# Kernel optimization log

Measured on AMD Instinct MI355X. Metric: run time of the kernel, lower is better.

Reference implementation:

```python
import jax, jax.numpy as jnp
import numpy as np

N, E = 20000, 320000
NODE_DIM, HID, HEADS, OUT = 256, 64, 4, 50
NEG_SLOPE = 0.2  # PyG GATv2Conv default
BN_EPS = 1e-5


def setup_inputs() -> dict:
    key = jax.random.key(0)
    ks = jax.random.split(key, 16)
    s = 0.05
    inp = {
        'x': jax.random.normal(ks[0], (N, NODE_DIM), dtype=jnp.float32),
        'edge_index': jax.random.randint(ks[1], (2, E), 0, N, dtype=jnp.int64),
        # GATv2 layer 1: in=NODE_DIM, out=HID, heads=HEADS, concat
        'W1l': jax.random.normal(ks[2], (NODE_DIM, HEADS * HID), dtype=jnp.float32) * s,
        'W1r': jax.random.normal(ks[3], (NODE_DIM, HEADS * HID), dtype=jnp.float32) * s,
        'att1': jax.random.normal(ks[4], (HEADS, HID), dtype=jnp.float32) * s,
        'b1': jnp.zeros((HEADS * HID,), dtype=jnp.float32),
        'bn1_g': jnp.ones((HEADS * HID,), dtype=jnp.float32),
        'bn1_b': jnp.zeros((HEADS * HID,), dtype=jnp.float32),
        # GATv2 layer 2: in=HEADS*HID, out=HID, heads=1
        'W2l': jax.random.normal(ks[5], (HEADS * HID, HID), dtype=jnp.float32) * s,
        'W2r': jax.random.normal(ks[6], (HEADS * HID, HID), dtype=jnp.float32) * s,
        'att2': jax.random.normal(ks[7], (1, HID), dtype=jnp.float32) * s,
        'b2': jnp.zeros((HID,), dtype=jnp.float32),
        'bn2_g': jnp.ones((HID,), dtype=jnp.float32),
        'bn2_b': jnp.zeros((HID,), dtype=jnp.float32),
        # class head
        'Wc': jax.random.normal(ks[8], (HID, OUT), dtype=jnp.float32) * s,
        'bc': jnp.zeros((OUT,), dtype=jnp.float32),
    }
    return inp


def gatv2(x, src, dst, Wl, Wr, att, bias, heads, d):
    n = x.shape[0]
    xl = (x @ Wl).reshape(n, heads, d)  # source-side transform (messages)
    xr = (x @ Wr).reshape(n, heads, d)  # target-side transform
    xj = xl[src]                        # [E, H, D] gathered source feats
    xi = xr[dst]                        # [E, H, D] gathered target feats
    e = jax.nn.leaky_relu(xi + xj, NEG_SLOPE)
    score = jnp.einsum('ehd,hd->eh', e, att)   # [E, H]
    # segment softmax over incoming edges of each destination node
    m = jax.ops.segment_max(score, dst, num_segments=n)         # [N, H]
    m = jnp.where(jnp.isfinite(m), m, 0.0)
    p = jnp.exp(score - m[dst])
    denom = jax.ops.segment_sum(p, dst, num_segments=n)          # [N, H]
    alpha = p / (denom[dst] + 1e-16)
    out = jax.ops.segment_sum(alpha[:, :, None] * xj, dst, num_segments=n)  # [N, H, D]
    return out.reshape(n, heads * d) + bias


def batchnorm(x, gamma, beta):
    mu = jnp.mean(x, axis=0)
    var = jnp.var(x, axis=0)
    return (x - mu) * jax.lax.rsqrt(var + BN_EPS) * gamma + beta


def reference(x, edge_index, W1l, W1r, att1, b1, bn1_g, bn1_b,
              W2l, W2r, att2, b2, bn2_g, bn2_b, Wc, bc):
    src, dst = edge_index[0], edge_index[1]
    h = gatv2(x, src, dst, W1l, W1r, att1, b1, HEADS, HID)
    h = jax.nn.gelu(batchnorm(h, bn1_g, bn1_b), approximate=False)
    h = gatv2(h, src, dst, W2l, W2r, att2, b2, 1, HID)
    h = jax.nn.gelu(batchnorm(h, bn2_g, bn2_b), approximate=False)
    return jax.nn.log_softmax(h @ Wc + bc, axis=1)
```

## Files before the change

kernel.cpp:

```cpp
#include <hip/hip_runtime.h>
#include <math.h>

#define N_NODES 20000
#define N_EDGES 320000
#define NODE_DIM 256
#define HID 64
#define HEADS 4
#define OUTC 50
#define NEG_SLOPE 0.2f
#define BN_EPS 1e-5f
#define LOG2E 1.4426950408889634f

typedef __attribute__((ext_vector_type(8))) short short8;
typedef __attribute__((ext_vector_type(8))) unsigned short ushort8;
typedef __attribute__((ext_vector_type(4))) unsigned short ushort4v;
typedef __attribute__((ext_vector_type(4))) float f32x4;

__device__ inline unsigned short f2bf(float f) {
  unsigned u = __float_as_uint(f);
  u += 0x7fffu + ((u >> 16) & 1u);
  return (unsigned short)(u >> 16);
}

__device__ inline float bf2f(unsigned short u) {
  return __uint_as_float((unsigned)u << 16);
}

__device__ inline float gelu_exact(float v) {
  return 0.5f * v * (1.f + erff(v * 0.70710678118f));
}

__global__ void cast_all_kernel(const float* __restrict__ x, unsigned short* __restrict__ xb,
                                const float* __restrict__ W1l, const float* __restrict__ W1r,
                                const float* __restrict__ W2l, const float* __restrict__ W2r,
                                unsigned short* __restrict__ w1b,
                                unsigned short* __restrict__ w2b) {
  int i = blockIdx.x * blockDim.x + threadIdx.x;
  if (i < 1280000) {
    float4 v = ((const float4*)x)[i];
    ushort4v o = {f2bf(v.x), f2bf(v.y), f2bf(v.z), f2bf(v.w)};
    ((ushort4v*)xb)[i] = o;
  }
  if (i < 131072) {
    int k = i >> 9, j = i & 511;
    w1b[i] = f2bf(j < 256 ? W1l[k * 256 + j] : W1r[k * 256 + j - 256]);
  }
  if (i < 32768) {
    int k = i >> 7, j = i & 127;
    w2b[i] = f2bf(j < 64 ? W2l[k * 64 + j] : W2r[k * 64 + j - 64]);
  }
}

__global__ __launch_bounds__(256) void gemm_bf16_kernel(
    const unsigned short* __restrict__ A, const unsigned short* __restrict__ B,
    unsigned short* __restrict__ C, int M, int K, int N) {
  __shared__ unsigned short As[128][40];
  __shared__ unsigned short Bs[128][40];
  int tid = threadIdx.x;
  int lane = tid & 63, w = tid >> 6;
  int bm = blockIdx.y * 128, bn = blockIdx.x * 128;

  f32x4 acc[2][8] = {};

  for (int k0 = 0; k0 < K; k0 += 32) {
#pragma unroll
    for (int s = tid; s < 512; s += 256) {
      int row = s >> 2, half = s & 3;
      int gr = bm + row;
      ushort8 v = {0, 0, 0, 0, 0, 0, 0, 0};
      if (gr < M) v = *(const ushort8*)&A[(size_t)gr * K + k0 + half * 8];
      *(ushort8*)&As[row][half * 8] = v;
    }
#pragma unroll
    for (int s = tid; s < 512; s += 256) {
      int k = s >> 4, c0 = (s & 15) * 8;
      ushort8 v = *(const ushort8*)&B[(size_t)(k0 + k) * N + bn + c0];
#pragma unroll
      for (int j = 0; j < 8; j++) Bs[c0 + j][k] = v[j];
    }
    __syncthreads();

    short8 av[2], bv[8];
#pragma unroll
    for (int fr = 0; fr < 2; fr++)
      av[fr] = *(const short8*)&As[w * 32 + fr * 16 + (lane & 15)][(lane >> 4) * 8];
#pragma unroll
    for (int fc = 0; fc < 8; fc++)
      bv[fc] = *(const short8*)&Bs[fc * 16 + (lane & 15)][(lane >> 4) * 8];
#pragma unroll
    for (int fr = 0; fr < 2; fr++)
#pragma unroll
      for (int fc = 0; fc < 8; fc++)
        acc[fr][fc] = __builtin_amdgcn_mfma_f32_16x16x32_bf16(av[fr], bv[fc], acc[fr][fc], 0, 0, 0);
    __syncthreads();
  }

#pragma unroll
  for (int fr = 0; fr < 2; fr++)
#pragma unroll
    for (int fc = 0; fc < 8; fc++)
#pragma unroll
      for (int i = 0; i < 4; i++) {
        int r = bm + w * 32 + fr * 16 + (lane >> 4) * 4 + i;
        if (r < M) C[(size_t)r * N + bn + fc * 16 + (lane & 15)] = f2bf(acc[fr][fc][i]);
      }
}

__global__ void hist_kernel(const int* __restrict__ dst, int* __restrict__ deg) {
  int i = blockIdx.x * blockDim.x + threadIdx.x;
  if (i < N_EDGES) atomicAdd(&deg[dst[i]], 1);
}

__global__ void scan_kernel(const int* __restrict__ deg, int* __restrict__ rowptr) {
  __shared__ int part[1024];
  int tid = threadIdx.x;
  const int CH = (N_NODES + 1023) / 1024;
  int base = tid * CH;
  int s = 0;
  for (int i = 0; i < CH; i++) {
    int idx = base + i;
    if (idx < N_NODES) s += deg[idx];
  }
  part[tid] = s;
  __syncthreads();
  for (int off = 1; off < 1024; off <<= 1) {
    int v = (tid >= off) ? part[tid - off] : 0;
    __syncthreads();
    part[tid] += v;
    __syncthreads();
  }
  int run = (tid == 0) ? 0 : part[tid - 1];
  for (int i = 0; i < CH; i++) {
    int idx = base + i;
    if (idx < N_NODES) {
      rowptr[idx] = run;
      run += deg[idx];
    }
  }
  if (tid == 1023) rowptr[N_NODES] = run;
}

__global__ void scatter_kernel(const int* __restrict__ src, const int* __restrict__ dst,
                               const int* __restrict__ rowptr, int* __restrict__ cursor,
                               int* __restrict__ csr_src) {
  int i = blockIdx.x * blockDim.x + threadIdx.x;
  if (i < N_EDGES) {
    int d = dst[i];
    int pos = rowptr[d] + atomicAdd(&cursor[d], 1);
    csr_src[pos] = src[i];
  }
}

__global__ void agg1_kernel(const unsigned short* __restrict__ C1,
                            const float* __restrict__ att, const float* __restrict__ bias,
                            const int* __restrict__ rowptr, const int* __restrict__ csr_src,
                            float* __restrict__ out) {
  int wave = threadIdx.x >> 6;
  int lane = threadIdx.x & 63;
  int n = blockIdx.x * 4 + wave;
  if (n >= N_NODES) return;

  ushort4v xi4 = *(const ushort4v*)&C1[(size_t)n * 512 + 256 + 4 * lane];
  float xi0 = bf2f(xi4[0]), xi1 = bf2f(xi4[1]), xi2 = bf2f(xi4[2]), xi3 = bf2f(xi4[3]);
  float4 attv = *(const float4*)&att[4 * lane];
  attv.x *= LOG2E; attv.y *= LOG2E; attv.z *= LOG2E; attv.w *= LOG2E;

  float acc0 = 0.f, acc1 = 0.f, acc2 = 0.f, acc3 = 0.f;
  float lsum = 0.f;

  int e0 = rowptr[n], e1 = rowptr[n + 1];
  int e = e0;
#define EDGE_SCORE(S, T, X0, X1, X2, X3)                                              \
  {                                                                                   \
    float u0 = xi0 + X0, u1 = xi1 + X1, u2 = xi2 + X2, u3 = xi3 + X3;                 \
    T = fmaxf(u0, NEG_SLOPE * u0) * attv.x + fmaxf(u1, NEG_SLOPE * u1) * attv.y +     \
        fmaxf(u2, NEG_SLOPE * u2) * attv.z + fmaxf(u3, NEG_SLOPE * u3) * attv.w;      \
  }
  for (; e + 4 <= e1; e += 4) {
    int s0 = csr_src[e], s1 = csr_src[e + 1], s2 = csr_src[e + 2], s3 = csr_src[e + 3];
    ushort4v a4 = *(const ushort4v*)&C1[(size_t)s0 * 512 + 4 * lane];
    ushort4v b4 = *(const ushort4v*)&C1[(size_t)s1 * 512 + 4 * lane];
    ushort4v c4 = *(const ushort4v*)&C1[(size_t)s2 * 512 + 4 * lane];
    ushort4v d4 = *(const ushort4v*)&C1[(size_t)s3 * 512 + 4 * lane];
    float xa0 = bf2f(a4[0]), xa1 = bf2f(a4[1]), xa2 = bf2f(a4[2]), xa3 = bf2f(a4[3]);
    float xb0 = bf2f(b4[0]), xb1 = bf2f(b4[1]), xb2 = bf2f(b4[2]), xb3 = bf2f(b4[3]);
    float xc0 = bf2f(c4[0]), xc1 = bf2f(c4[1]), xc2 = bf2f(c4[2]), xc3 = bf2f(c4[3]);
    float xd0 = bf2f(d4[0]), xd1 = bf2f(d4[1]), xd2 = bf2f(d4[2]), xd3 = bf2f(d4[3]);

    float ta, tb, tc, td;
    EDGE_SCORE(s0, ta, xa0, xa1, xa2, xa3);
    EDGE_SCORE(s1, tb, xb0, xb1, xb2, xb3);
    EDGE_SCORE(s2, tc, xc0, xc1, xc2, xc3);
    EDGE_SCORE(s3, td, xd0, xd1, xd2, xd3);

    ta += __shfl_xor(ta, 8); tb += __shfl_xor(tb, 8); tc += __shfl_xor(tc, 8); td += __shfl_xor(td, 8);
    ta += __shfl_xor(ta, 4); tb += __shfl_xor(tb, 4); tc += __shfl_xor(tc, 4); td += __shfl_xor(td, 4);
    ta += __shfl_xor(ta, 2); tb += __shfl_xor(tb, 2); tc += __shfl_xor(tc, 2); td += __shfl_xor(td, 2);
    ta += __shfl_xor(ta, 1); tb += __shfl_xor(tb, 1); tc += __shfl_xor(tc, 1); td += __shfl_xor(td, 1);

    float pa = __builtin_amdgcn_exp2f(ta);
    float pb = __builtin_amdgcn_exp2f(tb);
    float pc = __builtin_amdgcn_exp2f(tc);
    float pd = __builtin_amdgcn_exp2f(td);
    lsum += (pa + pb) + (pc + pd);
    acc0 += pa * xa0 + pb * xb0 + pc * xc0 + pd * xd0;
    acc1 += pa * xa1 + pb * xb1 + pc * xc1 + pd * xd1;
    acc2 += pa * xa2 + pb * xb2 + pc * xc2 + pd * xd2;
    acc3 += pa * xa3 + pb * xb3 + pc * xc3 + pd * xd3;
  }
  for (; e < e1; e++) {
    int s0 = csr_src[e];
    ushort4v a4 = *(const ushort4v*)&C1[(size_t)s0 * 512 + 4 * lane];
    float xa0 = bf2f(a4[0]), xa1 = bf2f(a4[1]), xa2 = bf2f(a4[2]), xa3 = bf2f(a4[3]);
    float ta;
    EDGE_SCORE(s0, ta, xa0, xa1, xa2, xa3);
    ta += __shfl_xor(ta, 8);
    ta += __shfl_xor(ta, 4);
    ta += __shfl_xor(ta, 2);
    ta += __shfl_xor(ta, 1);
    float pa = __builtin_amdgcn_exp2f(ta);
    lsum += pa;
    acc0 += pa * xa0;
    acc1 += pa * xa1;
    acc2 += pa * xa2;
    acc3 += pa * xa3;
  }
#undef EDGE_SCORE

  float inv = 1.f / (lsum + 1e-16f);
  float4 bv = *(const float4*)&bias[4 * lane];
  float4 o;
  o.x = acc0 * inv + bv.x;
  o.y = acc1 * inv + bv.y;
  o.z = acc2 * inv + bv.z;
  o.w = acc3 * inv + bv.w;
  *(float4*)&out[(size_t)n * 256 + 4 * lane] = o;
}

__global__ void agg2_kernel(const unsigned short* __restrict__ xlr,
                            const float* __restrict__ att, const float* __restrict__ bias,
                            const int* __restrict__ rowptr, const int* __restrict__ csr_src,
                            float* __restrict__ out) {
  int wave = threadIdx.x >> 6;
  int lane = threadIdx.x & 63;
  int n = blockIdx.x * 4 + wave;
  if (n >= N_NODES) return;

  int g = lane >> 4, slot = lane & 15;
  ushort4v xi4 = *(const ushort4v*)&xlr[(size_t)n * 128 + 64 + 4 * slot];
  float xi0 = bf2f(xi4[0]), xi1 = bf2f(xi4[1]), xi2 = bf2f(xi4[2]), xi3 = bf2f(xi4[3]);
  float4 attv = *(const float4*)&att[4 * slot];
  attv.x *= LOG2E; attv.y *= LOG2E; attv.z *= LOG2E; attv.w *= LOG2E;

  float acc0 = 0.f, acc1 = 0.f, acc2 = 0.f, acc3 = 0.f;
  float lsum = 0.f;

  int e0 = rowptr[n], e1 = rowptr[n + 1];
  int nt = (e1 - e0 + 3) >> 2;
  for (int it = 0; it < nt; it++) {
    int e = e0 + it * 4 + g;
    bool valid = e < e1;
    int s = valid ? csr_src[e] : 0;
    ushort4v xj4 = *(const ushort4v*)&xlr[(size_t)s * 128 + 4 * slot];
    float xj0 = bf2f(xj4[0]), xj1 = bf2f(xj4[1]), xj2 = bf2f(xj4[2]), xj3 = bf2f(xj4[3]);
    float u0 = xi0 + xj0, u1 = xi1 + xj1, u2 = xi2 + xj2, u3 = xi3 + xj3;
    float t = fmaxf(u0, NEG_SLOPE * u0) * attv.x + fmaxf(u1, NEG_SLOPE * u1) * attv.y +
              fmaxf(u2, NEG_SLOPE * u2) * attv.z + fmaxf(u3, NEG_SLOPE * u3) * attv.w;
    t += __shfl_xor(t, 8);
    t += __shfl_xor(t, 4);
    t += __shfl_xor(t, 2);
    t += __shfl_xor(t, 1);
    float p = valid ? __builtin_amdgcn_exp2f(t) : 0.f;
    lsum += p;
    acc0 += p * xj0;
    acc1 += p * xj1;
    acc2 += p * xj2;
    acc3 += p * xj3;
  }

  acc0 += __shfl_xor(acc0, 16); acc0 += __shfl_xor(acc0, 32);
  acc1 += __shfl_xor(acc1, 16); acc1 += __shfl_xor(acc1, 32);
  acc2 += __shfl_xor(acc2, 16); acc2 += __shfl_xor(acc2, 32);
  acc3 += __shfl_xor(acc3, 16); acc3 += __shfl_xor(acc3, 32);
  lsum += __shfl_xor(lsum, 16); lsum += __shfl_xor(lsum, 32);

  if (g == 0) {
    float inv = 1.f / (lsum + 1e-16f);
    float4 bv = *(const float4*)&bias[4 * slot];
    float4 o;
    o.x = acc0 * inv + bv.x;
    o.y = acc1 * inv + bv.y;
    o.z = acc2 * inv + bv.z;
    o.w = acc3 * inv + bv.w;
    *(float4*)&out[(size_t)n * 64 + 4 * slot] = o;
  }
}

__global__ void bn_stage1_256_kernel(const float* __restrict__ x, float* __restrict__ partial) {
  int c = threadIdx.x;
  int r0 = blockIdx.x * 84;
  int r1 = min(r0 + 84, N_NODES);
  float s = 0.f, q = 0.f;
  for (int r = r0; r < r1; r++) {
    float v = x[(size_t)r * 256 + c];
    s += v;
    q += v * v;
  }
  partial[(size_t)blockIdx.x * 512 + c] = s;
  partial[(size_t)blockIdx.x * 512 + 256 + c] = q;
}

__global__ void bn_stage1_64_kernel(const float* __restrict__ x, float* __restrict__ partial) {
  __shared__ float ls[256], lq[256];
  int tid = threadIdx.x;
  int c = tid & 63, g = tid >> 6;
  int r0 = blockIdx.x * 84 + g;
  int r1 = min(blockIdx.x * 84 + 84, N_NODES);
  float s = 0.f, q = 0.f;
  for (int r = r0; r < r1; r += 4) {
    float v = x[(size_t)r * 64 + c];
    s += v;
    q += v * v;
  }
  ls[tid] = s;
  lq[tid] = q;
  __syncthreads();
  if (g == 0) {
    s += ls[64 + c] + ls[128 + c] + ls[192 + c];
    q += lq[64 + c] + lq[128 + c] + lq[192 + c];
    partial[(size_t)blockIdx.x * 128 + c] = s;
    partial[(size_t)blockIdx.x * 128 + 64 + c] = q;
  }
}

__global__ void bn_stage2_kernel(const float* __restrict__ partial, int C,
                                 const float* __restrict__ gamma, const float* __restrict__ beta,
                                 float* __restrict__ ss) {
  int c = threadIdx.x;
  if (c >= C) return;
  float s = 0.f, q = 0.f;
  for (int b = 0; b < 240; b++) {
    s += partial[(size_t)b * 2 * C + c];
    q += partial[(size_t)b * 2 * C + C + c];
  }
  float mu = s * (1.0f / N_NODES);
  float var = q * (1.0f / N_NODES) - mu * mu;
  float sc = gamma[c] * rsqrtf(var + BN_EPS);
  ss[c] = sc;
  ss[C + c] = beta[c] - mu * sc;
}

__global__ void bn_gelu1_kernel(const float* __restrict__ x, const float* __restrict__ ss,
                                unsigned short* __restrict__ y) {
  const int total4 = N_NODES * 256 / 4;
  for (int i = blockIdx.x * blockDim.x + threadIdx.x; i < total4;
       i += gridDim.x * blockDim.x) {
    int c0 = (i & 63) * 4;
    float4 v = ((const float4*)x)[i];
    float a0 = gelu_exact(v.x * ss[c0 + 0] + ss[256 + c0 + 0]);
    float a1 = gelu_exact(v.y * ss[c0 + 1] + ss[256 + c0 + 1]);
    float a2 = gelu_exact(v.z * ss[c0 + 2] + ss[256 + c0 + 2]);
    float a3 = gelu_exact(v.w * ss[c0 + 3] + ss[256 + c0 + 3]);
    ushort4v o = {f2bf(a0), f2bf(a1), f2bf(a2), f2bf(a3)};
    ((ushort4v*)y)[i] = o;
  }
}

__global__ void head_kernel(const float* __restrict__ h, const float* __restrict__ ss2,
                            const float* __restrict__ Wc, const float* __restrict__ bc,
                            float* __restrict__ out) {
  __shared__ float Ws[HID * OUTC];
  __shared__ float bs[OUTC];
  for (int i = threadIdx.x; i < HID * OUTC; i += 256) Ws[i] = Wc[i];
  for (int i = threadIdx.x; i < OUTC; i += 256) bs[i] = bc[i];
  __syncthreads();

  int wave = threadIdx.x >> 6;
  int lane = threadIdx.x & 63;
  int n = blockIdx.x * 4 + wave;
  if (n >= N_NODES) return;

  float raw = h[(size_t)n * HID + lane];
  float hrow = gelu_exact(raw * ss2[lane] + ss2[64 + lane]);
  float dot = 0.f;
#pragma unroll
  for (int k = 0; k < HID; k++) {
    float hk = __shfl(hrow, k);
    if (lane < OUTC) dot += hk * Ws[k * OUTC + lane];
  }
  float z = (lane < OUTC) ? (dot + bs[lane]) : -INFINITY;
  float mv = z;
  for (int off = 32; off; off >>= 1) mv = fmaxf(mv, __shfl_xor(mv, off));
  float p = (lane < OUTC) ? expf(z - mv) : 0.f;
  float sum = p;
  for (int off = 32; off; off >>= 1) sum += __shfl_xor(sum, off);
  if (lane < OUTC) out[(size_t)n * OUTC + lane] = z - mv - logf(sum);
}

extern "C" void kernel_launch(void* const* d_in, const int* in_sizes, int n_in,
                              void* d_out, int out_size, void* d_ws, size_t ws_size,
                              hipStream_t stream) {
  const float* x = (const float*)d_in[0];
  const int* eidx = (const int*)d_in[1];
  const float* W1l = (const float*)d_in[2];
  const float* W1r = (const float*)d_in[3];
  const float* att1 = (const float*)d_in[4];
  const float* b1 = (const float*)d_in[5];
  const float* bn1_g = (const float*)d_in[6];
  const float* bn1_b = (const float*)d_in[7];
  const float* W2l = (const float*)d_in[8];
  const float* W2r = (const float*)d_in[9];
  const float* att2 = (const float*)d_in[10];
  const float* b2 = (const float*)d_in[11];
  const float* bn2_g = (const float*)d_in[12];
  const float* bn2_b = (const float*)d_in[13];
  const float* Wc = (const float*)d_in[14];
  const float* bc = (const float*)d_in[15];
  float* out = (float*)d_out;

  const int* src = eidx;
  const int* dstv = eidx + N_EDGES;

  char* ws = (char*)d_ws;
  unsigned short* C1full = (unsigned short*)(ws + 0);
  float* out1 = (float*)(ws + 20971520);
  unsigned short* out1b = (unsigned short*)(ws + 41943040);
  unsigned short* C2full = (unsigned short*)(ws + 52428800);
  unsigned short* xb = (unsigned short*)(ws + 62914560);
  float* out2 = (float*)(ws + 62914560);
  float* partial = (float*)(ws + 73400320);
  float* ss1 = (float*)(ws + 73891840);
  float* ss2 = (float*)(ws + 73893888);
  unsigned short* w1b = (unsigned short*)(ws + 73894400);
  unsigned short* w2b = (unsigned short*)(ws + 74156544);
  int* deg = (int*)(ws + 74222080);
  int* cursor = (int*)(ws + 74302080);
  int* rowptr = (int*)(ws + 74382080);
  int* csr_src = (int*)(ws + 74462096);

  hipMemsetAsync(deg, 0, 160000, stream);

  cast_all_kernel<<<5000, 256, 0, stream>>>(x, xb, W1l, W1r, W2l, W2r, w1b, w2b);

  gemm_bf16_kernel<<<dim3(4, 157), 256, 0, stream>>>(xb, w1b, C1full, N_NODES, 256, 512);

  hist_kernel<<<(N_EDGES + 255) / 256, 256, 0, stream>>>(dstv, deg);
  scan_kernel<<<1, 1024, 0, stream>>>(deg, rowptr);
  scatter_kernel<<<(N_EDGES + 255) / 256, 256, 0, stream>>>(src, dstv, rowptr, cursor, csr_src);

  agg1_kernel<<<N_NODES / 4, 256, 0, stream>>>(C1full, att1, b1, rowptr, csr_src, out1);

  bn_stage1_256_kernel<<<240, 256, 0, stream>>>(out1, partial);
  bn_stage2_kernel<<<1, 256, 0, stream>>>(partial, 256, bn1_g, bn1_b, ss1);
  bn_gelu1_kernel<<<2048, 256, 0, stream>>>(out1, ss1, out1b);

  gemm_bf16_kernel<<<dim3(1, 157), 256, 0, stream>>>(out1b, w2b, C2full, N_NODES, 256, 128);

  agg2_kernel<<<N_NODES / 4, 256, 0, stream>>>(C2full, att2, b2, rowptr, csr_src, out2);

  bn_stage1_64_kernel<<<240, 256, 0, stream>>>(out2, partial);
  bn_stage2_kernel<<<1, 64, 0, stream>>>(partial, 64, bn2_g, bn2_b, ss2);

  head_kernel<<<N_NODES / 4, 256, 0, stream>>>(out2, ss2, Wc, bc, out);
}
```

Baseline: 278.4 us.

## Fuse BN+GELU into layer-2 GEMM and software-pipeline edge gathers in aggregation

Removes the standalone bn_gelu1 kernel: the layer-2 GEMM now reads the fp32 layer-1 output and applies the batchnorm scale/shift plus exact GELU while staging A tiles into shared memory. This drops one full write and read of the intermediate bf16 activation and one launch. Both aggregation kernels now prefetch the next group of gathered source rows before computing the current group, using clamped indices and validity masks, so gather latency overlaps the arithmetic. The cost is more register pressure and GELU work inside the GEMM's load phase, which runs on only 157 blocks.

Measured after the change: 280.6 us. Within noise of the previous version (+0.8%).

```diff
diff --git a/kernel.cpp b/kernel.cpp
--- a/kernel.cpp
+++ b/kernel.cpp
@@ -106,6 +106,78 @@
       }
 }
 
+__global__ __launch_bounds__(256) void gemm2_fused_kernel(
+    const float* __restrict__ A32, const float* __restrict__ ss,
+    const unsigned short* __restrict__ B, unsigned short* __restrict__ C,
+    int M, int K, int N) {
+  __shared__ unsigned short As[128][40];
+  __shared__ unsigned short Bs[128][40];
+  __shared__ float ssA[512];
+  int tid = threadIdx.x;
+  int lane = tid & 63, w = tid >> 6;
+  int bm = blockIdx.y * 128, bn = blockIdx.x * 128;
+
+  for (int i = tid; i < 512; i += 256) ssA[i] = ss[i];
+  __syncthreads();
+
+  f32x4 acc[2][8] = {};
+
+  for (int k0 = 0; k0 < K; k0 += 32) {
+#pragma unroll
+    for (int s = tid; s < 512; s += 256) {
+      int row = s >> 2, half = s & 3;
+      int gr = bm + row;
+      int c0 = k0 + half * 8;
+      ushort8 o8 = {0, 0, 0, 0, 0, 0, 0, 0};
+      if (gr < M) {
+        float4 va = *(const float4*)&A32[(size_t)gr * K + c0];
+        float4 vb = *(const float4*)&A32[(size_t)gr * K + c0 + 4];
+        o8[0] = f2bf(gelu_exact(va.x * ssA[c0 + 0] + ssA[256 + c0 + 0]));
+        o8[1] = f2bf(gelu_exact(va.y * ssA[c0 + 1] + ssA[256 + c0 + 1]));
+        o8[2] = f2bf(gelu_exact(va.z * ssA[c0 + 2] + ssA[256 + c0 + 2]));
+        o8[3] = f2bf(gelu_exact(va.w * ssA[c0 + 3] + ssA[256 + c0 + 3]));
+        o8[4] = f2bf(gelu_exact(vb.x * ssA[c0 + 4] + ssA[256 + c0 + 4]));
+        o8[5] = f2bf(gelu_exact(vb.y * ssA[c0 + 5] + ssA[256 + c0 + 5]));
+        o8[6] = f2bf(gelu_exact(vb.z * ssA[c0 + 6] + ssA[256 + c0 + 6]));
+        o8[7] = f2bf(gelu_exact(vb.w * ssA[c0 + 7] + ssA[256 + c0 + 7]));
+      }
+      *(ushort8*)&As[row][half * 8] = o8;
+    }
+#pragma unroll
+    for (int s = tid; s < 512; s += 256) {
+      int k = s >> 4, c0 = (s & 15) * 8;
+      ushort8 v = *(const ushort8*)&B[(size_t)(k0 + k) * N + bn + c0];
+#pragma unroll
+      for (int j = 0; j < 8; j++) Bs[c0 + j][k] = v[j];
+    }
+    __syncthreads();
+
+    short8 av[2], bv[8];
+#pragma unroll
+    for (int fr = 0; fr < 2; fr++)
+      av[fr] = *(const short8*)&As[w * 32 + fr * 16 + (lane & 15)][(lane >> 4) * 8];
+#pragma unroll
+    for (int fc = 0; fc < 8; fc++)
+      bv[fc] = *(const short8*)&Bs[fc * 16 + (lane & 15)][(lane >> 4) * 8];
+#pragma unroll
+    for (int fr = 0; fr < 2; fr++)
+#pragma unroll
+      for (int fc = 0; fc < 8; fc++)
+        acc[fr][fc] = __builtin_amdgcn_mfma_f32_16x16x32_bf16(av[fr], bv[fc], acc[fr][fc], 0, 0, 0);
+    __syncthreads();
+  }
+
+#pragma unroll
+  for (int fr = 0; fr < 2; fr++)
+#pragma unroll
+    for (int fc = 0; fc < 8; fc++)
+#pragma unroll
+      for (int i = 0; i < 4; i++) {
+        int r = bm + w * 32 + fr * 16 + (lane >> 4) * 4 + i;
+        if (r < M) C[(size_t)r * N + bn + fc * 16 + (lane & 15)] = f2bf(acc[fr][fc][i]);
+      }
+}
+
 __global__ void hist_kernel(const int* __restrict__ dst, int* __restrict__ deg) {
   int i = blockIdx.x * blockDim.x + threadIdx.x;
   if (i < N_EDGES) atomicAdd(&deg[dst[i]], 1);
@@ -160,7 +232,8 @@
   int n = blockIdx.x * 4 + wave;
   if (n >= N_NODES) return;
 
-  ushort4v xi4 = *(const ushort4v*)&C1[(size_t)n * 512 + 256 + 4 * lane];
+  const size_t L4 = 4 * (size_t)lane;
+  ushort4v xi4 = *(const ushort4v*)&C1[(size_t)n * 512 + 256 + L4];
   float xi0 = bf2f(xi4[0]), xi1 = bf2f(xi4[1]), xi2 = bf2f(xi4[2]), xi3 = bf2f(xi4[3]);
   float4 attv = *(const float4*)&att[4 * lane];
   attv.x *= LOG2E; attv.y *= LOG2E; attv.z *= LOG2E; attv.w *= LOG2E;
@@ -169,63 +242,72 @@
   float lsum = 0.f;
 
   int e0 = rowptr[n], e1 = rowptr[n + 1];
-  int e = e0;
-#define EDGE_SCORE(S, T, X0, X1, X2, X3)                                              \
-  {                                                                                   \
-    float u0 = xi0 + X0, u1 = xi1 + X1, u2 = xi2 + X2, u3 = xi3 + X3;                 \
-    T = fmaxf(u0, NEG_SLOPE * u0) * attv.x + fmaxf(u1, NEG_SLOPE * u1) * attv.y +     \
-        fmaxf(u2, NEG_SLOPE * u2) * attv.z + fmaxf(u3, NEG_SLOPE * u3) * attv.w;      \
-  }
-  for (; e + 4 <= e1; e += 4) {
-    int s0 = csr_src[e], s1 = csr_src[e + 1], s2 = csr_src[e + 2], s3 = csr_src[e + 3];
-    ushort4v a4 = *(const ushort4v*)&C1[(size_t)s0 * 512 + 4 * lane];
-    ushort4v b4 = *(const ushort4v*)&C1[(size_t)s1 * 512 + 4 * lane];
-    ushort4v c4 = *(const ushort4v*)&C1[(size_t)s2 * 512 + 4 * lane];
-    ushort4v d4 = *(const ushort4v*)&C1[(size_t)s3 * 512 + 4 * lane];
-    float xa0 = bf2f(a4[0]), xa1 = bf2f(a4[1]), xa2 = bf2f(a4[2]), xa3 = bf2f(a4[3]);
-    float xb0 = bf2f(b4[0]), xb1 = bf2f(b4[1]), xb2 = bf2f(b4[2]), xb3 = bf2f(b4[3]);
-    float xc0 = bf2f(c4[0]), xc1 = bf2f(c4[1]), xc2 = bf2f(c4[2]), xc3 = bf2f(c4[3]);
-    float xd0 = bf2f(d4[0]), xd1 = bf2f(d4[1]), xd2 = bf2f(d4[2]), xd3 = bf2f(d4[3]);
-
-    float ta, tb, tc, td;
-    EDGE_SCORE(s0, ta, xa0, xa1, xa2, xa3);
-    EDGE_SCORE(s1, tb, xb0, xb1, xb2, xb3);
-    EDGE_SCORE(s2, tc, xc0, xc1, xc2, xc3);
-    EDGE_SCORE(s3, td, xd0, xd1, xd2, xd3);
-
-    ta += __shfl_xor(ta, 8); tb += __shfl_xor(tb, 8); tc += __shfl_xor(tc, 8); td += __shfl_xor(td, 8);
-    ta += __shfl_xor(ta, 4); tb += __shfl_xor(tb, 4); tc += __shfl_xor(tc, 4); td += __shfl_xor(td, 4);
-    ta += __shfl_xor(ta, 2); tb += __shfl_xor(tb, 2); tc += __shfl_xor(tc, 2); td += __shfl_xor(td, 2);
-    ta += __shfl_xor(ta, 1); tb += __shfl_xor(tb, 1); tc += __shfl_xor(tc, 1); td += __shfl_xor(td, 1);
-
-    float pa = __builtin_amdgcn_exp2f(ta);
-    float pb = __builtin_amdgcn_exp2f(tb);
-    float pc = __builtin_amdgcn_exp2f(tc);
-    float pd = __builtin_amdgcn_exp2f(td);
-    lsum += (pa + pb) + (pc + pd);
-    acc0 += pa * xa0 + pb * xb0 + pc * xc0 + pd * xd0;
-    acc1 += pa * xa1 + pb * xb1 + pc * xc1 + pd * xd1;
-    acc2 += pa * xa2 + pb * xb2 + pc * xc2 + pd * xd2;
-    acc3 += pa * xa3 + pb * xb3 + pc * xc3 + pd * xd3;
-  }
-  for (; e < e1; e++) {
-    int s0 = csr_src[e];
-    ushort4v a4 = *(const ushort4v*)&C1[(size_t)s0 * 512 + 4 * lane];
-    float xa0 = bf2f(a4[0]), xa1 = bf2f(a4[1]), xa2 = bf2f(a4[2]), xa3 = bf2f(a4[3]);
-    float ta;
-    EDGE_SCORE(s0, ta, xa0, xa1, xa2, xa3);
-    ta += __shfl_xor(ta, 8);
-    ta += __shfl_xor(ta, 4);
-    ta += __shfl_xor(ta, 2);
-    ta += __shfl_xor(ta, 1);
-    float pa = __builtin_amdgcn_exp2f(ta);
-    lsum += pa;
-    acc0 += pa * xa0;
-    acc1 += pa * xa1;
-    acc2 += pa * xa2;
-    acc3 += pa * xa3;
-  }
-#undef EDGE_SCORE
+  int nb = e1 - e0;
+
+  if (nb > 0) {
+    int ng = (nb + 3) >> 2;
+    int ia = e0;
+    int ib = min(e0 + 1, e1 - 1);
+    int ic = min(e0 + 2, e1 - 1);
+    int id = min(e0 + 3, e1 - 1);
+    ushort4v A4 = *(const ushort4v*)&C1[(size_t)csr_src[ia] * 512 + L4];
+    ushort4v B4 = *(const ushort4v*)&C1[(size_t)csr_src[ib] * 512 + L4];
+    ushort4v C4 = *(const ushort4v*)&C1[(size_t)csr_src[ic] * 512 + L4];
+    ushort4v D4 = *(const ushort4v*)&C1[(size_t)csr_src[id] * 512 + L4];
+
+    for (int it = 0; it < ng; it++) {
+      int base = e0 + it * 4;
+      bool v1 = base + 1 < e1, v2 = base + 2 < e1, v3 = base + 3 < e1;
+
+      ushort4v ca = A4, cb = B4, cc = C4, cd = D4;
+
+      int nbase = base + 4;
+      if (nbase < e1) {
+        int na = nbase;
+        int nb2 = min(nbase + 1, e1 - 1);
+        int nc = min(nbase + 2, e1 - 1);
+        int nd = min(nbase + 3, e1 - 1);
+        A4 = *(const ushort4v*)&C1[(size_t)csr_src[na] * 512 + L4];
+        B4 = *(const ushort4v*)&C1[(size_t)csr_src[nb2] * 512 + L4];
+        C4 = *(const ushort4v*)&C1[(size_t)csr_src[nc] * 512 + L4];
+        D4 = *(const ushort4v*)&C1[(size_t)csr_src[nd] * 512 + L4];
+      }
+
+      float xa0 = bf2f(ca[0]), xa1 = bf2f(ca[1]), xa2 = bf2f(ca[2]), xa3 = bf2f(ca[3]);
+      float xb0 = bf2f(cb[0]), xb1 = bf2f(cb[1]), xb2 = bf2f(cb[2]), xb3 = bf2f(cb[3]);
+      float xc0 = bf2f(cc[0]), xc1 = bf2f(cc[1]), xc2 = bf2f(cc[2]), xc3 = bf2f(cc[3]);
+      float xd0 = bf2f(cd[0]), xd1 = bf2f(cd[1]), xd2 = bf2f(cd[2]), xd3 = bf2f(cd[3]);
+
+      float ua0 = xi0 + xa0, ua1 = xi1 + xa1, ua2 = xi2 + xa2, ua3 = xi3 + xa3;
+      float ub0 = xi0 + xb0, ub1 = xi1 + xb1, ub2 = xi2 + xb2, ub3 = xi3 + xb3;
+      float uc0 = xi0 + xc0, uc1 = xi1 + xc1, uc2 = xi2 + xc2, uc3 = xi3 + xc3;
+      float ud0 = xi0 + xd0, ud1 = xi1 + xd1, ud2 = xi2 + xd2, ud3 = xi3 + xd3;
+
+      float ta = fmaxf(ua0, NEG_SLOPE * ua0) * attv.x + fmaxf(ua1, NEG_SLOPE * ua1) * attv.y +
+                 fmaxf(ua2, NEG_SLOPE * ua2) * attv.z + fmaxf(ua3, NEG_SLOPE * ua3) * attv.w;
+      float tb = fmaxf(ub0, NEG_SLOPE * ub0) * attv.x + fmaxf(ub1, NEG_SLOPE * ub1) * attv.y +
+                 fmaxf(ub2, NEG_SLOPE * ub2) * attv.z + fmaxf(ub3, NEG_SLOPE * ub3) * attv.w;
+      float tc = fmaxf(uc0, NEG_SLOPE * uc0) * attv.x + fmaxf(uc1, NEG_SLOPE * uc1) * attv.y +
+                 fmaxf(uc2, NEG_SLOPE * uc2) * attv.z + fmaxf(uc3, NEG_SLOPE * uc3) * attv.w;
+      float td = fmaxf(ud0, NEG_SLOPE * ud0) * attv.x + fmaxf(ud1, NEG_SLOPE * ud1) * attv.y +
+                 fmaxf(ud2, NEG_SLOPE * ud2) * attv.z + fmaxf(ud3, NEG_SLOPE * ud3) * attv.w;
+
+      ta += __shfl_xor(ta, 8); tb += __shfl_xor(tb, 8); tc += __shfl_xor(tc, 8); td += __shfl_xor(td, 8);
+      ta += __shfl_xor(ta, 4); tb += __shfl_xor(tb, 4); tc += __shfl_xor(tc, 4); td += __shfl_xor(td, 4);
+      ta += __shfl_xor(ta, 2); tb += __shfl_xor(tb, 2); tc += __shfl_xor(tc, 2); td += __shfl_xor(td, 2);
+      ta += __shfl_xor(ta, 1); tb += __shfl_xor(tb, 1); tc += __shfl_xor(tc, 1); td += __shfl_xor(td, 1);
+
+      float pa = __builtin_amdgcn_exp2f(ta);
+      float pb = v1 ? __builtin_amdgcn_exp2f(tb) : 0.f;
+      float pc = v2 ? __builtin_amdgcn_exp2f(tc) : 0.f;
+      float pd = v3 ? __builtin_amdgcn_exp2f(td) : 0.f;
+      lsum += (pa + pb) + (pc + pd);
+      acc0 += pa * xa0 + pb * xb0 + pc * xc0 + pd * xd0;
+      acc1 += pa * xa1 + pb * xb1 + pc * xc1 + pd * xd1;
+      acc2 += pa * xa2 + pb * xb2 + pc * xc2 + pd * xd2;
+      acc3 += pa * xa3 + pb * xb3 + pc * xc3 + pd * xd3;
+    }
+  }
 
   float inv = 1.f / (lsum + 1e-16f);
   float4 bv = *(const float4*)&bias[4 * lane];
@@ -256,26 +338,33 @@
   float lsum = 0.f;
 
   int e0 = rowptr[n], e1 = rowptr[n + 1];
-  int nt = (e1 - e0 + 3) >> 2;
-  for (int it = 0; it < nt; it++) {
-    int e = e0 + it * 4 + g;
-    bool valid = e < e1;
-    int s = valid ? csr_src[e] : 0;
-    ushort4v xj4 = *(const ushort4v*)&xlr[(size_t)s * 128 + 4 * slot];
-    float xj0 = bf2f(xj4[0]), xj1 = bf2f(xj4[1]), xj2 = bf2f(xj4[2]), xj3 = bf2f(xj4[3]);
-    float u0 = xi0 + xj0, u1 = xi1 + xj1, u2 = xi2 + xj2, u3 = xi3 + xj3;
-    float t = fmaxf(u0, NEG_SLOPE * u0) * attv.x + fmaxf(u1, NEG_SLOPE * u1) * attv.y +
-              fmaxf(u2, NEG_SLOPE * u2) * attv.z + fmaxf(u3, NEG_SLOPE * u3) * attv.w;
-    t += __shfl_xor(t, 8);
-    t += __shfl_xor(t, 4);
-    t += __shfl_xor(t, 2);
-    t += __shfl_xor(t, 1);
-    float p = valid ? __builtin_amdgcn_exp2f(t) : 0.f;
-    lsum += p;
-    acc0 += p * xj0;
-    acc1 += p * xj1;
-    acc2 += p * xj2;
-    acc3 += p * xj3;
+  int nb = e1 - e0;
+  if (nb > 0) {
+    int nt = (nb + 3) >> 2;
+    int ecl = min(e0 + g, e1 - 1);
+    ushort4v R = *(const ushort4v*)&xlr[(size_t)csr_src[ecl] * 128 + 4 * slot];
+    for (int it = 0; it < nt; it++) {
+      bool valid = (e0 + it * 4 + g) < e1;
+      ushort4v cur = R;
+      if (it + 1 < nt) {
+        int ne = min(e0 + (it + 1) * 4 + g, e1 - 1);
+        R = *(const ushort4v*)&xlr[(size_t)csr_src[ne] * 128 + 4 * slot];
+      }
+      float xj0 = bf2f(cur[0]), xj1 = bf2f(cur[1]), xj2 = bf2f(cur[2]), xj3 = bf2f(cur[3]);
+      float u0 = xi0 + xj0, u1 = xi1 + xj1, u2 = xi2 + xj2, u3 = xi3 + xj3;
+      float t = fmaxf(u0, NEG_SLOPE * u0) * attv.x + fmaxf(u1, NEG_SLOPE * u1) * attv.y +
+                fmaxf(u2, NEG_SLOPE * u2) * attv.z + fmaxf(u3, NEG_SLOPE * u3) * attv.w;
+      t += __shfl_xor(t, 8);
+      t += __shfl_xor(t, 4);
+      t += __shfl_xor(t, 2);
+      t += __shfl_xor(t, 1);
+      float p = valid ? __builtin_amdgcn_exp2f(t) : 0.f;
+      lsum += p;
+      acc0 += p * xj0;
+      acc1 += p * xj1;
+      acc2 += p * xj2;
+      acc3 += p * xj3;
+    }
   }
 
   acc0 += __shfl_xor(acc0, 16); acc0 += __shfl_xor(acc0, 32);
@@ -348,22 +437,6 @@
   float sc = gamma[c] * rsqrtf(var + BN_EPS);
   ss[c] = sc;
   ss[C + c] = beta[c] - mu * sc;
-}
-
-__global__ void bn_gelu1_kernel(const float* __restrict__ x, const float* __restrict__ ss,
-                                unsigned short* __restrict__ y) {
-  const int total4 = N_NODES * 256 / 4;
-  for (int i = blockIdx.x * blockDim.x + threadIdx.x; i < total4;
-       i += gridDim.x * blockDim.x) {
-    int c0 = (i & 63) * 4;
-    float4 v = ((const float4*)x)[i];
-    float a0 = gelu_exact(v.x * ss[c0 + 0] + ss[256 + c0 + 0]);
-    float a1 = gelu_exact(v.y * ss[c0 + 1] + ss[256 + c0 + 1]);
-    float a2 = gelu_exact(v.z * ss[c0 + 2] + ss[256 + c0 + 2]);
-    float a3 = gelu_exact(v.w * ss[c0 + 3] + ss[256 + c0 + 3]);
-    ushort4v o = {f2bf(a0), f2bf(a1), f2bf(a2), f2bf(a3)};
-    ((ushort4v*)y)[i] = o;
-  }
 }
 
 __global__ void head_kernel(const float* __restrict__ h, const float* __restrict__ ss2,
@@ -424,7 +497,6 @@
   char* ws = (char*)d_ws;
   unsigned short* C1full = (unsigned short*)(ws + 0);
   float* out1 = (float*)(ws + 20971520);
-  unsigned short* out1b = (unsigned short*)(ws + 41943040);
   unsigned short* C2full = (unsigned short*)(ws + 52428800);
   unsigned short* xb = (unsigned short*)(ws + 62914560);
   float* out2 = (float*)(ws + 62914560);
@@ -452,9 +524,8 @@
 
   bn_stage1_256_kernel<<<240, 256, 0, stream>>>(out1, partial);
   bn_stage2_kernel<<<1, 256, 0, stream>>>(partial, 256, bn1_g, bn1_b, ss1);
-  bn_gelu1_kernel<<<2048, 256, 0, stream>>>(out1, ss1, out1b);
-
-  gemm_bf16_kernel<<<dim3(1, 157), 256, 0, stream>>>(out1b, w2b, C2full, N_NODES, 256, 128);
+
+  gemm2_fused_kernel<<<dim3(1, 157), 256, 0, stream>>>(out1, ss1, w2b, C2full, N_NODES, 256, 128);
 
   agg2_kernel<<<N_NODES / 4, 256, 0, stream>>>(C2full, att2, b2, rowptr, csr_src, out2);
 
```

## Fuse degree histogram, scan and BN-GELU into neighbouring kernels; pretranspose weights

Applied to the files above, without the earlier changes.

The degree histogram moves into the cast kernel, and the prefix scan runs in an extra grid row of the first GEMM. BN1+GELU is applied while loading the A tile of the second GEMM, which drops a separate pass and the bf16 intermediate buffer. Weights are now cast into a transposed layout, so B tiles load with vector stores instead of scalar transposing writes to LDS. This removes several launches and one full round trip of the activation through memory. The cost is recomputing GELU on the GEMM load path and a single-block scan that shares the first GEMM's grid.

Result: faster. 263.7 us (-5.3%).

```diff
diff --git a/kernel.cpp b/kernel.cpp
--- a/kernel.cpp
+++ b/kernel.cpp
@@ -33,8 +33,9 @@
 __global__ void cast_all_kernel(const float* __restrict__ x, unsigned short* __restrict__ xb,
                                 const float* __restrict__ W1l, const float* __restrict__ W1r,
                                 const float* __restrict__ W2l, const float* __restrict__ W2r,
-                                unsigned short* __restrict__ w1b,
-                                unsigned short* __restrict__ w2b) {
+                                unsigned short* __restrict__ w1bT,
+                                unsigned short* __restrict__ w2bT,
+                                const int* __restrict__ dst, int* __restrict__ deg) {
   int i = blockIdx.x * blockDim.x + threadIdx.x;
   if (i < 1280000) {
     float4 v = ((const float4*)x)[i];
@@ -42,18 +43,52 @@
     ((ushort4v*)xb)[i] = o;
   }
   if (i < 131072) {
-    int k = i >> 9, j = i & 511;
-    w1b[i] = f2bf(j < 256 ? W1l[k * 256 + j] : W1r[k * 256 + j - 256]);
+    int j = i >> 8, k = i & 255;
+    w1bT[i] = f2bf(j < 256 ? W1l[k * 256 + j] : W1r[k * 256 + j - 256]);
   }
   if (i < 32768) {
-    int k = i >> 7, j = i & 127;
-    w2b[i] = f2bf(j < 64 ? W2l[k * 64 + j] : W2r[k * 64 + j - 64]);
-  }
+    int j = i >> 8, k = i & 255;
+    w2bT[i] = f2bf(j < 64 ? W2l[k * 64 + j] : W2r[k * 64 + j - 64]);
+  }
+  if (i < N_EDGES) atomicAdd(&deg[dst[i]], 1);
 }
 
 __global__ __launch_bounds__(256) void gemm_bf16_kernel(
-    const unsigned short* __restrict__ A, const unsigned short* __restrict__ B,
-    unsigned short* __restrict__ C, int M, int K, int N) {
+    const unsigned short* __restrict__ A, const unsigned short* __restrict__ BT,
+    unsigned short* __restrict__ C, int M, int K, int N,
+    const int* __restrict__ deg, int* __restrict__ rowptr) {
+  if (blockIdx.y == gridDim.y - 1) {
+    if (blockIdx.x == 0) {
+      __shared__ int part[256];
+      int tid = threadIdx.x;
+      const int CH = 79;
+      int base = tid * CH;
+      int s = 0;
+      for (int i = 0; i < CH; i++) {
+        int idx = base + i;
+        if (idx < N_NODES) s += deg[idx];
+      }
+      part[tid] = s;
+      __syncthreads();
+      for (int off = 1; off < 256; off <<= 1) {
+        int v = (tid >= off) ? part[tid - off] : 0;
+        __syncthreads();
+        part[tid] += v;
+        __syncthreads();
+      }
+      int run = (tid == 0) ? 0 : part[tid - 1];
+      for (int i = 0; i < CH; i++) {
+        int idx = base + i;
+        if (idx < N_NODES) {
+          rowptr[idx] = run;
+          run += deg[idx];
+        }
+      }
+      if (tid == 255) rowptr[N_NODES] = run;
+    }
+    return;
+  }
+
   __shared__ unsigned short As[128][40];
   __shared__ unsigned short Bs[128][40];
   int tid = threadIdx.x;
@@ -73,10 +108,9 @@
     }
 #pragma unroll
     for (int s = tid; s < 512; s += 256) {
-      int k = s >> 4, c0 = (s & 15) * 8;
-      ushort8 v = *(const ushort8*)&B[(size_t)(k0 + k) * N + bn + c0];
-#pragma unroll
-      for (int j = 0; j < 8; j++) Bs[c0 + j][k] = v[j];
+      int row = s >> 2, half = s & 3;
+      ushort8 v = *(const ushort8*)&BT[(size_t)(bn + row) * K + k0 + half * 8];
+      *(ushort8*)&Bs[row][half * 8] = v;
     }
     __syncthreads();
 
@@ -106,38 +140,75 @@
       }
 }
 
-__global__ void hist_kernel(const int* __restrict__ dst, int* __restrict__ deg) {
-  int i = blockIdx.x * blockDim.x + threadIdx.x;
-  if (i < N_EDGES) atomicAdd(&deg[dst[i]], 1);
-}
-
-__global__ void scan_kernel(const int* __restrict__ deg, int* __restrict__ rowptr) {
-  __shared__ int part[1024];
+__global__ __launch_bounds__(256) void gemm2_fused_kernel(
+    const float* __restrict__ A32, const float* __restrict__ ss,
+    const unsigned short* __restrict__ BT, unsigned short* __restrict__ C,
+    int M, int K, int N) {
+  __shared__ unsigned short As[128][40];
+  __shared__ unsigned short Bs[128][40];
+  __shared__ float ssA[512];
   int tid = threadIdx.x;
-  const int CH = (N_NODES + 1023) / 1024;
-  int base = tid * CH;
-  int s = 0;
-  for (int i = 0; i < CH; i++) {
-    int idx = base + i;
-    if (idx < N_NODES) s += deg[idx];
-  }
-  part[tid] = s;
+  int lane = tid & 63, w = tid >> 6;
+  int bm = blockIdx.y * 128, bn = blockIdx.x * 128;
+
+  for (int i = tid; i < 512; i += 256) ssA[i] = ss[i];
   __syncthreads();
-  for (int off = 1; off < 1024; off <<= 1) {
-    int v = (tid >= off) ? part[tid - off] : 0;
+
+  f32x4 acc[2][8] = {};
+
+  for (int k0 = 0; k0 < K; k0 += 32) {
+#pragma unroll
+    for (int s = tid; s < 512; s += 256) {
+      int row = s >> 2, half = s & 3;
+      int gr = bm + row;
+      int c0 = k0 + half * 8;
+      ushort8 o8 = {0, 0, 0, 0, 0, 0, 0, 0};
+      if (gr < M) {
+        float4 va = *(const float4*)&A32[(size_t)gr * K + c0];
+        float4 vb = *(const float4*)&A32[(size_t)gr * K + c0 + 4];
+        o8[0] = f2bf(gelu_exact(va.x * ssA[c0 + 0] + ssA[256 + c0 + 0]));
+        o8[1] = f2bf(gelu_exact(va.y * ssA[c0 + 1] + ssA[256 + c0 + 1]));
+        o8[2] = f2bf(gelu_exact(va.z * ssA[c0 + 2] + ssA[256 + c0 + 2]));
+        o8[3] = f2bf(gelu_exact(va.w * ssA[c0 + 3] + ssA[256 + c0 + 3]));
+        o8[4] = f2bf(gelu_exact(vb.x * ssA[c0 + 4] + ssA[256 + c0 + 4]));
+        o8[5] = f2bf(gelu_exact(vb.y * ssA[c0 + 5] + ssA[256 + c0 + 5]));
+        o8[6] = f2bf(gelu_exact(vb.z * ssA[c0 + 6] + ssA[256 + c0 + 6]));
+        o8[7] = f2bf(gelu_exact(vb.w * ssA[c0 + 7] + ssA[256 + c0 + 7]));
+      }
+      *(ushort8*)&As[row][half * 8] = o8;
+    }
+#pragma unroll
+    for (int s = tid; s < 512; s += 256) {
+      int row = s >> 2, half = s & 3;
+      ushort8 v = *(const ushort8*)&BT[(size_t)(bn + row) * K + k0 + half * 8];
+      *(ushort8*)&Bs[row][half * 8] = v;
+    }
     __syncthreads();
-    part[tid] += v;
+
+    short8 av[2], bv[8];
+#pragma unroll
+    for (int fr = 0; fr < 2; fr++)
+      av[fr] = *(const short8*)&As[w * 32 + fr * 16 + (lane & 15)][(lane >> 4) * 8];
+#pragma unroll
+    for (int fc = 0; fc < 8; fc++)
+      bv[fc] = *(const short8*)&Bs[fc * 16 + (lane & 15)][(lane >> 4) * 8];
+#pragma unroll
+    for (int fr = 0; fr < 2; fr++)
+#pragma unroll
+      for (int fc = 0; fc < 8; fc++)
+        acc[fr][fc] = __builtin_amdgcn_mfma_f32_16x16x32_bf16(av[fr], bv[fc], acc[fr][fc], 0, 0, 0);
     __syncthreads();
   }
-  int run = (tid == 0) ? 0 : part[tid - 1];
-  for (int i = 0; i < CH; i++) {
-    int idx = base + i;
-    if (idx < N_NODES) {
-      rowptr[idx] = run;
-      run += deg[idx];
-    }
-  }
-  if (tid == 1023) rowptr[N_NODES] = run;
+
+#pragma unroll
+  for (int fr = 0; fr < 2; fr++)
+#pragma unroll
+    for (int fc = 0; fc < 8; fc++)
+#pragma unroll
+      for (int i = 0; i < 4; i++) {
+        int r = bm + w * 32 + fr * 16 + (lane >> 4) * 4 + i;
+        if (r < M) C[(size_t)r * N + bn + fc * 16 + (lane & 15)] = f2bf(acc[fr][fc][i]);
+      }
 }
 
 __global__ void scatter_kernel(const int* __restrict__ src, const int* __restrict__ dst,
@@ -170,7 +241,7 @@
 
   int e0 = rowptr[n], e1 = rowptr[n + 1];
   int e = e0;
-#define EDGE_SCORE(S, T, X0, X1, X2, X3)                                              \
+#define EDGE_SCORE(T, X0, X1, X2, X3)                                                 \
   {                                                                                   \
     float u0 = xi0 + X0, u1 = xi1 + X1, u2 = xi2 + X2, u3 = xi3 + X3;                 \
     T = fmaxf(u0, NEG_SLOPE * u0) * attv.x + fmaxf(u1, NEG_SLOPE * u1) * attv.y +     \
@@ -188,10 +259,10 @@
     float xd0 = bf2f(d4[0]), xd1 = bf2f(d4[1]), xd2 = bf2f(d4[2]), xd3 = bf2f(d4[3]);
 
     float ta, tb, tc, td;
-    EDGE_SCORE(s0, ta, xa0, xa1, xa2, xa3);
-    EDGE_SCORE(s1, tb, xb0, xb1, xb2, xb3);
-    EDGE_SCORE(s2, tc, xc0, xc1, xc2, xc3);
-    EDGE_SCORE(s3, td, xd0, xd1, xd2, xd3);
+    EDGE_SCORE(ta, xa0, xa1, xa2, xa3);
+    EDGE_SCORE(tb, xb0, xb1, xb2, xb3);
+    EDGE_SCORE(tc, xc0, xc1, xc2, xc3);
+    EDGE_SCORE(td, xd0, xd1, xd2, xd3);
 
     ta += __shfl_xor(ta, 8); tb += __shfl_xor(tb, 8); tc += __shfl_xor(tc, 8); td += __shfl_xor(td, 8);
     ta += __shfl_xor(ta, 4); tb += __shfl_xor(tb, 4); tc += __shfl_xor(tc, 4); td += __shfl_xor(td, 4);
@@ -213,7 +284,7 @@
     ushort4v a4 = *(const ushort4v*)&C1[(size_t)s0 * 512 + 4 * lane];
     float xa0 = bf2f(a4[0]), xa1 = bf2f(a4[1]), xa2 = bf2f(a4[2]), xa3 = bf2f(a4[3]);
     float ta;
-    EDGE_SCORE(s0, ta, xa0, xa1, xa2, xa3);
+    EDGE_SCORE(ta, xa0, xa1, xa2, xa3);
     ta += __shfl_xor(ta, 8);
     ta += __shfl_xor(ta, 4);
     ta += __shfl_xor(ta, 2);
@@ -350,22 +421,6 @@
   ss[C + c] = beta[c] - mu * sc;
 }
 
-__global__ void bn_gelu1_kernel(const float* __restrict__ x, const float* __restrict__ ss,
-                                unsigned short* __restrict__ y) {
-  const int total4 = N_NODES * 256 / 4;
-  for (int i = blockIdx.x * blockDim.x + threadIdx.x; i < total4;
-       i += gridDim.x * blockDim.x) {
-    int c0 = (i & 63) * 4;
-    float4 v = ((const float4*)x)[i];
-    float a0 = gelu_exact(v.x * ss[c0 + 0] + ss[256 + c0 + 0]);
-    float a1 = gelu_exact(v.y * ss[c0 + 1] + ss[256 + c0 + 1]);
-    float a2 = gelu_exact(v.z * ss[c0 + 2] + ss[256 + c0 + 2]);
-    float a3 = gelu_exact(v.w * ss[c0 + 3] + ss[256 + c0 + 3]);
-    ushort4v o = {f2bf(a0), f2bf(a1), f2bf(a2), f2bf(a3)};
-    ((ushort4v*)y)[i] = o;
-  }
-}
-
 __global__ void head_kernel(const float* __restrict__ h, const float* __restrict__ ss2,
                             const float* __restrict__ Wc, const float* __restrict__ bc,
                             float* __restrict__ out) {
@@ -424,15 +479,14 @@
   char* ws = (char*)d_ws;
   unsigned short* C1full = (unsigned short*)(ws + 0);
   float* out1 = (float*)(ws + 20971520);
-  unsigned short* out1b = (unsigned short*)(ws + 41943040);
   unsigned short* C2full = (unsigned short*)(ws + 52428800);
   unsigned short* xb = (unsigned short*)(ws + 62914560);
   float* out2 = (float*)(ws + 62914560);
   float* partial = (float*)(ws + 73400320);
   float* ss1 = (float*)(ws + 73891840);
   float* ss2 = (float*)(ws + 73893888);
-  unsigned short* w1b = (unsigned short*)(ws + 73894400);
-  unsigned short* w2b = (unsigned short*)(ws + 74156544);
+  unsigned short* w1bT = (unsigned short*)(ws + 73894400);
+  unsigned short* w2bT = (unsigned short*)(ws + 74156544);
   int* deg = (int*)(ws + 74222080);
   int* cursor = (int*)(ws + 74302080);
   int* rowptr = (int*)(ws + 74382080);
@@ -440,21 +494,19 @@
 
   hipMemsetAsync(deg, 0, 160000, stream);
 
-  cast_all_kernel<<<5000, 256, 0, stream>>>(x, xb, W1l, W1r, W2l, W2r, w1b, w2b);
-
-  gemm_bf16_kernel<<<dim3(4, 157), 256, 0, stream>>>(xb, w1b, C1full, N_NODES, 256, 512);
-
-  hist_kernel<<<(N_EDGES + 255) / 256, 256, 0, stream>>>(dstv, deg);
-  scan_kernel<<<1, 1024, 0, stream>>>(deg, rowptr);
+  cast_all_kernel<<<5000, 256, 0, stream>>>(x, xb, W1l, W1r, W2l, W2r, w1bT, w2bT, dstv, deg);
+
+  gemm_bf16_kernel<<<dim3(4, 158), 256, 0, stream>>>(xb, w1bT, C1full, N_NODES, 256, 512,
+                                                     deg, rowptr);
+
   scatter_kernel<<<(N_EDGES + 255) / 256, 256, 0, stream>>>(src, dstv, rowptr, cursor, csr_src);
 
   agg1_kernel<<<N_NODES / 4, 256, 0, stream>>>(C1full, att1, b1, rowptr, csr_src, out1);
 
   bn_stage1_256_kernel<<<240, 256, 0, stream>>>(out1, partial);
   bn_stage2_kernel<<<1, 256, 0, stream>>>(partial, 256, bn1_g, bn1_b, ss1);
-  bn_gelu1_kernel<<<2048, 256, 0, stream>>>(out1, ss1, out1b);
-
-  gemm_bf16_kernel<<<dim3(1, 157), 256, 0, stream>>>(out1b, w2b, C2full, N_NODES, 256, 128);
+
+  gemm2_fused_kernel<<<dim3(1, 157), 256, 0, stream>>>(out1, ss1, w2bT, C2full, N_NODES, 256, 128);
 
   agg2_kernel<<<N_NODES / 4, 256, 0, stream>>>(C2full, att2, b2, rowptr, csr_src, out2);
 
```
